# Optimization experiments

Hardware: AMD Instinct MI355X
Metric: run time of the kernel (lower is better)

Reference implementation:

```python
import jax, jax.numpy as jnp
import numpy as np

B, T, C, H = 8, 2048, 1024, 128

def setup_inputs() -> dict:
    key = jax.random.key(0)
    k1, k2, k3, k4 = jax.random.split(key, 4)
    scale = C ** -0.5  # init scale for weights, roughly matches nn.Linear default magnitude
    return {
        "x": jax.random.normal(k1, (B, T, C), dtype=jnp.float32),
        "Wk": jax.random.normal(k2, (C, H), dtype=jnp.float32) * scale,
        "Wq": jax.random.normal(k3, (C, H), dtype=jnp.float32) * scale,
        "Wv": jax.random.normal(k4, (C, H), dtype=jnp.float32) * scale,
    }

def reference(x, Wk, Wq, Wv):
    # x: [B, T, C]; W*: [C, H] (torch Linear weight transposed, bias=False)
    Bx, Tx, Cx = x.shape
    k = x @ Wk  # [B, T, H]
    q = x @ Wq  # [B, T, H]
    v = x @ Wv  # [B, T, H]
    # NOTE: original scales by C**(-0.5) (embedding size), not head_size**-0.5
    scores = jnp.einsum('bth,bsh->bts', q, k) * (Cx ** -0.5)  # [B, T, T]
    causal = jnp.tril(jnp.ones((Tx, Tx), dtype=bool))
    scores = jnp.where(causal, scores, -jnp.inf)
    w = jax.nn.softmax(scores, axis=-1)  # dropout is identity in eval mode
    out = jnp.einsum('bts,bsh->bth', w, v)  # [B, T, H]
    return out
```

## Files before the change

kernel.cpp:

```cpp
#include <hip/hip_runtime.h>


typedef __attribute__((ext_vector_type(8))) short short8;
typedef __attribute__((ext_vector_type(4))) float f32x4;

typedef const __attribute__((address_space(1))) unsigned int* gas_u32p;
typedef __attribute__((address_space(3))) unsigned int* las_u32p;

static __device__ __forceinline__ unsigned short f2bf(float f) {
  unsigned int u = __float_as_uint(f);
  u += 0x7FFF + ((u >> 16) & 1);
  return (unsigned short)(u >> 16);
}

__global__ void wtrans_kernel(const float* __restrict__ Wq,
                              const float* __restrict__ Wk,
                              const float* __restrict__ Wv,
                              unsigned short* __restrict__ Wt) {
  int idx = blockIdx.x * blockDim.x + threadIdx.x;
  int C  = idx >> 3;
  int e  = idx & 7;
  int l  = C & 63;
  int t1 = C >> 6;
  int kh = t1 & 1;
  int t2 = t1 >> 1;
  int w  = t2 % 3;
  int t3 = t2 / 3;
  int wave = t3 & 7;
  int kt   = t3 >> 3;
  int n = wave * 16 + (l & 15);
  int k = kt * 64 + kh * 32 + (l >> 4) * 8 + e;
  const float* W = (w == 0) ? Wq : (w == 1) ? Wk : Wv;
  Wt[idx] = f2bf(W[k * 128 + n]);
}

__global__ __launch_bounds__(512) void qkv_kernel(
    const float* __restrict__ x,
    const unsigned short* __restrict__ Wt,
    unsigned short* __restrict__ q,
    unsigned short* __restrict__ kb,
    unsigned short* __restrict__ vt)
{
  __shared__ float xl[4][4096];
  const int tid  = threadIdx.x;
  const int lane = tid & 63;
  const int wave = tid >> 6;
  const int m0   = blockIdx.x * 64;
  const int lr   = lane & 15;

  f32x4 acc[4][3];
  #pragma unroll
  for (int i = 0; i < 4; ++i)
    #pragma unroll
    for (int w = 0; w < 3; ++w) acc[i][w] = (f32x4){0.f, 0.f, 0.f, 0.f};

  int srow[2], skq[2];
  #pragma unroll
  for (int i = 0; i < 2; ++i) {
    int c  = i * 512 + tid;
    int ln = c & 63;
    int g  = c >> 6;
    srow[i] = (g >> 2) * 16 + (ln & 15);
    skq[i]  = ((g >> 1) & 1) * 8 + (ln >> 4) * 2 + (g & 1);
  }

  #define QSTAGE(KT, BUF)                                                        \
    do {                                                                         \
      _Pragma("unroll")                                                          \
      for (int i = 0; i < 2; ++i) {                                              \
        const float* gsrc = x + (size_t)(m0 + srow[i]) * 1024 + (KT) * 64 + skq[i] * 4; \
        __builtin_amdgcn_global_load_lds((gas_u32p)gsrc,                         \
            (las_u32p)&xl[BUF][(i * 512 + tid) * 4], 16, 0, 0);                  \
      }                                                                          \
    } while (0)

  const unsigned short* w2base = Wt + wave * 3072 + lane * 8;

  #define WLOAD(KT, DST)                                                         \
    do {                                                                         \
      _Pragma("unroll")                                                          \
      for (int w = 0; w < 3; ++w) {                                              \
        DST[w][0] = *reinterpret_cast<const short8*>(w2base + (KT) * 24576 + w * 1024);       \
        DST[w][1] = *reinterpret_cast<const short8*>(w2base + (KT) * 24576 + w * 1024 + 512); \
      }                                                                          \
    } while (0)

  short8 wbuf[2][3][2];

  WLOAD(0, wbuf[0]);
  QSTAGE(0, 0);
  QSTAGE(1, 1);

  #pragma unroll
  for (int kt = 0; kt < 16; ++kt) {
    if (kt < 15) WLOAD(kt + 1, wbuf[(kt + 1) & 1]);
    if (kt < 14) QSTAGE(kt + 2, (kt + 2) & 3);
    if (kt < 14)      asm volatile("s_waitcnt vmcnt(10)" ::: "memory");
    else if (kt < 15) asm volatile("s_waitcnt vmcnt(8)"  ::: "memory");
    else              asm volatile("s_waitcnt vmcnt(0)"  ::: "memory");
    __builtin_amdgcn_sched_barrier(0);
    __builtin_amdgcn_s_barrier();

    short8 af[4][2];
    #pragma unroll
    for (int mf = 0; mf < 4; ++mf)
      #pragma unroll
      for (int kh = 0; kh < 2; ++kh) {
        const float* basep = &xl[kt & 3][((mf * 2 + kh) * 2) * 256 + lane * 4];
        f32x4 h0 = *reinterpret_cast<const f32x4*>(basep);
        f32x4 h1 = *reinterpret_cast<const f32x4*>(basep + 256);
        union { unsigned int w[4]; short8 s; } cv;
        asm("v_cvt_pk_bf16_f32 %0, %1, %2" : "=v"(cv.w[0]) : "v"(h0[0]), "v"(h0[1]));
        asm("v_cvt_pk_bf16_f32 %0, %1, %2" : "=v"(cv.w[1]) : "v"(h0[2]), "v"(h0[3]));
        asm("v_cvt_pk_bf16_f32 %0, %1, %2" : "=v"(cv.w[2]) : "v"(h1[0]), "v"(h1[1]));
        asm("v_cvt_pk_bf16_f32 %0, %1, %2" : "=v"(cv.w[3]) : "v"(h1[2]), "v"(h1[3]));
        af[mf][kh] = cv.s;
      }

    __builtin_amdgcn_s_setprio(1);
    #pragma unroll
    for (int w = 0; w < 3; ++w)
      #pragma unroll
      for (int mf = 0; mf < 4; ++mf) {
        acc[mf][w] = __builtin_amdgcn_mfma_f32_16x16x32_bf16(af[mf][0], wbuf[kt & 1][w][0], acc[mf][w], 0, 0, 0);
        acc[mf][w] = __builtin_amdgcn_mfma_f32_16x16x32_bf16(af[mf][1], wbuf[kt & 1][w][1], acc[mf][w], 0, 0, 0);
      }
    __builtin_amdgcn_s_setprio(0);
  }
  #undef QSTAGE
  #undef WLOAD

  const int h = wave * 16 + lr;
  const int b = m0 >> 11;
  #pragma unroll
  for (int mf = 0; mf < 4; ++mf) {
    int r0 = m0 + mf * 16 + (lane >> 4) * 4;
    #pragma unroll
    for (int j = 0; j < 4; ++j) {
      int r = r0 + j;
      q[(size_t)r * 128 + h] = f2bf(acc[mf][0][j]);
      int rr  = r & 63;
      int nf  = ((rr >> 5) & 1) * 2 + ((rr >> 2) & 1);
      int lrk = ((rr >> 3) & 3) * 4 + (rr & 3);
      size_t kidx = (size_t)(r >> 6) * 8192
                  + (size_t)(((nf * 4 + (h >> 5)) * 64 + ((h >> 3) & 3) * 16 + lrk) * 8 + (h & 7));
      kb[kidx] = f2bf(acc[mf][1][j]);
    }
    int t = r0 & 2047;
    size_t vidx = (size_t)b * 262144 + (size_t)(t >> 6) * 8192
                + (size_t)(((((h >> 4) * 2 + ((t >> 5) & 1)) * 64 + ((t >> 3) & 3) * 16 + (h & 15)) * 8) + (t & 7));
    ushort4 u;
    u.x = f2bf(acc[mf][2][0]); u.y = f2bf(acc[mf][2][1]);
    u.z = f2bf(acc[mf][2][2]); u.w = f2bf(acc[mf][2][3]);
    *reinterpret_cast<ushort4*>(vt + vidx) = u;
  }
}

template<bool MASK>
static __device__ __forceinline__ void body_regs(
    int s, int myrow0, int myrow1, int lg,
    const short8 (&kf)[2][4], const short8 (&vf)[8],
    const short8 (&qf)[2][4], f32x4 (&o)[2][8], float (&lsum)[2])
{
  const float SC = 0.03125f * 1.44269504f;

  f32x4 sT[2][2];
  __builtin_amdgcn_s_setprio(1);
  #pragma unroll
  for (int g = 0; g < 2; ++g)
    #pragma unroll
    for (int nf = 0; nf < 2; ++nf) {
      sT[g][nf] = (f32x4){0.f, 0.f, 0.f, 0.f};
      #pragma unroll
      for (int ks = 0; ks < 4; ++ks)
        sT[g][nf] = __builtin_amdgcn_mfma_f32_16x16x32_bf16(kf[nf][ks], qf[g][ks], sT[g][nf], 0, 0, 0);
    }
  __builtin_amdgcn_s_setprio(0);

  union { unsigned int w[4]; short8 s8; } cv[2];
  #pragma unroll
  for (int g = 0; g < 2; ++g) {
    const int myrow = g ? myrow1 : myrow0;
    float p[8];
    #pragma unroll
    for (int nf = 0; nf < 2; ++nf)
      #pragma unroll
      for (int j = 0; j < 4; ++j) {
        float sv = sT[g][nf][j] * SC;
        if (MASK) {
          int kv = s * 32 + lg * 8 + nf * 4 + j;
          if (kv > myrow) sv = -1e30f;
        }
        p[nf * 4 + j] = exp2f(sv);
      }
    lsum[g] += ((p[0] + p[1]) + (p[2] + p[3])) + ((p[4] + p[5]) + (p[6] + p[7]));
    #pragma unroll
    for (int u = 0; u < 4; ++u)
      asm("v_cvt_pk_bf16_f32 %0, %1, %2" : "=v"(cv[g].w[u]) : "v"(p[u * 2]), "v"(p[u * 2 + 1]));
  }

  __builtin_amdgcn_s_setprio(1);
  #pragma unroll
  for (int g = 0; g < 2; ++g)
    #pragma unroll
    for (int n = 0; n < 8; ++n)
      o[g][n] = __builtin_amdgcn_mfma_f32_16x16x32_bf16(vf[n], cv[g].s8, o[g][n], 0, 0, 0);
  __builtin_amdgcn_s_setprio(0);
}

__global__ __launch_bounds__(256, 2) void attn_kernel(
    const unsigned short* __restrict__ q,
    const unsigned short* __restrict__ kb,
    const unsigned short* __restrict__ vt,
    float* __restrict__ out)
{
  __shared__ float mb[12672];

  const int tid  = threadIdx.x;
  const int lane = tid & 63;
  const int wv   = tid >> 6;
  const int lr = lane & 15;
  const int lg = lane >> 4;
  const int bid = blockIdx.x;
  const int b  = bid & 7;
  const int g2 = bid >> 3;
  const int tt = (g2 < 32) ? (63 - g2) : (g2 - 32);
  const int t0 = tt * 32;
  const int nb = tt + 1;

  const unsigned short* kbase = kb + (size_t)b * 262144;
  const unsigned short* vbase = vt + (size_t)b * 262144;
  const int myrow0 = t0 + lr;
  const int myrow1 = t0 + 16 + lr;

  short8 qf[2][4];
  #pragma unroll
  for (int g = 0; g < 2; ++g) {
    const unsigned short* qp = q + ((size_t)(b * 2048) + (g ? myrow1 : myrow0)) * 128 + lg * 8;
    #pragma unroll
    for (int ks = 0; ks < 4; ++ks)
      qf[g][ks] = *reinterpret_cast<const short8*>(qp + ks * 32);
  }

  f32x4 o[2][8];
  #pragma unroll
  for (int g = 0; g < 2; ++g)
    #pragma unroll
    for (int n = 0; n < 8; ++n) o[g][n] = (f32x4){0.f, 0.f, 0.f, 0.f};
  float lsum[2] = {0.f, 0.f};

  #define GLOADK(KF, S)                                                          \
    do {                                                                         \
      const unsigned short* kg = kbase + (size_t)((S) >> 1) * 8192 + ((S) & 1) * 4096; \
      _Pragma("unroll")                                                          \
      for (int nf = 0; nf < 2; ++nf)                                             \
        _Pragma("unroll")                                                        \
        for (int ks = 0; ks < 4; ++ks)                                           \
          KF[nf][ks] = *reinterpret_cast<const short8*>(kg + ((nf * 4 + ks) * 64 + lane) * 8); \
    } while (0)

  #define GLOADV(S)                                                              \
    do {                                                                         \
      const unsigned short* vg = vbase + (size_t)((S) >> 1) * 8192;              \
      const int hh = (S) & 1;                                                    \
      _Pragma("unroll")                                                          \
      for (int n = 0; n < 8; ++n)                                                \
        vf[n] = *reinterpret_cast<const short8*>(vg + ((n * 2 + hh) * 64 + lane) * 8); \
    } while (0)

  short8 kfA[2][4], kfB[2][4], vf[8];

  if (wv < nb) GLOADK(kfA, wv);

  #define PHASE(CURK, NXTK)                                                      \
    do {                                                                         \
      GLOADV(s);                                                                 \
      if (s + 4 < nb) GLOADK(NXTK, s + 4);                                       \
      if (s == nb - 1)                                                           \
        body_regs<true >(s, myrow0, myrow1, lg, CURK, vf, qf, o, lsum);          \
      else                                                                       \
        body_regs<false>(s, myrow0, myrow1, lg, CURK, vf, qf, o, lsum);          \
    } while (0)

  int s = wv;
  #pragma unroll 1
  while (s < nb) {
    PHASE(kfA, kfB);
    s += 4;
    if (s >= nb) break;
    PHASE(kfB, kfA);
    s += 4;
  }
  #undef PHASE
  #undef GLOADK
  #undef GLOADV

  __syncthreads();
  if (wv != 0) {
    #pragma unroll
    for (int g = 0; g < 2; ++g)
      #pragma unroll
      for (int n = 0; n < 8; ++n) {
        float4 st;
        st.x = o[g][n][0]; st.y = o[g][n][1]; st.z = o[g][n][2]; st.w = o[g][n][3];
        *reinterpret_cast<float4*>(&mb[(size_t)((wv - 1) * 16 + g * 8 + n) * 256 + lane * 4]) = st;
      }
    mb[12288 + (wv - 1) * 128 + lane]      = lsum[0];
    mb[12288 + (wv - 1) * 128 + 64 + lane] = lsum[1];
  }
  __syncthreads();
  if (wv == 0) {
    #pragma unroll
    for (int g = 0; g < 2; ++g) {
      #pragma unroll
      for (int n = 0; n < 8; ++n) {
        #pragma unroll
        for (int w = 1; w < 4; ++w) {
          float4 ad = *reinterpret_cast<const float4*>(
              &mb[(size_t)((w - 1) * 16 + g * 8 + n) * 256 + lane * 4]);
          o[g][n][0] += ad.x; o[g][n][1] += ad.y; o[g][n][2] += ad.z; o[g][n][3] += ad.w;
        }
      }
      float ps = lsum[g];
      #pragma unroll
      for (int w = 1; w < 4; ++w)
        ps += mb[12288 + (w - 1) * 128 + g * 64 + lane];
      ps += __shfl_xor(ps, 16);
      ps += __shfl_xor(ps, 32);
      float rcp = 1.0f / ps;
      float* op = out + ((size_t)(b * 2048) + (g ? myrow1 : myrow0)) * 128;
      #pragma unroll
      for (int n = 0; n < 8; ++n) {
        float4 st;
        st.x = o[g][n][0] * rcp; st.y = o[g][n][1] * rcp;
        st.z = o[g][n][2] * rcp; st.w = o[g][n][3] * rcp;
        *reinterpret_cast<float4*>(op + n * 16 + lg * 4) = st;
      }
    }
  }
}

extern "C" void kernel_launch(void* const* d_in, const int* in_sizes, int n_in,
                              void* d_out, int out_size, void* d_ws, size_t ws_size,
                              hipStream_t stream) {
  const float* x  = (const float*)d_in[0];
  const float* Wk = (const float*)d_in[1];
  const float* Wq = (const float*)d_in[2];
  const float* Wv = (const float*)d_in[3];
  float* out = (float*)d_out;

  char* ws = (char*)d_ws;
  unsigned short* q  = (unsigned short*)(ws);
  unsigned short* kb = (unsigned short*)(ws + (4u  << 20));
  unsigned short* vt = (unsigned short*)(ws + (8u  << 20));
  unsigned short* Wt = (unsigned short*)(ws + (12u << 20));

  wtrans_kernel<<<dim3(1536), dim3(256), 0, stream>>>(Wq, Wk, Wv, Wt);
  qkv_kernel<<<dim3(256), dim3(512), 0, stream>>>(x, Wt, q, kb, vt);
  attn_kernel<<<dim3(512), dim3(256), 0, stream>>>(q, kb, vt, out);
}
```

Before: 57.54 us.

## Process 64-key blocks per wave iteration and drop K double-buffer prefetch

```diff
diff --git a/kernel.cpp b/kernel.cpp
--- a/kernel.cpp
+++ b/kernel.cpp
@@ -157,19 +157,19 @@
 }
 
 template<bool MASK>
-static __device__ __forceinline__ void body_regs(
+static __device__ __forceinline__ void body64(
     int s, int myrow0, int myrow1, int lg,
-    const short8 (&kf)[2][4], const short8 (&vf)[8],
+    const short8 (&kf)[4][4], const short8 (&vf)[8][2],
     const short8 (&qf)[2][4], f32x4 (&o)[2][8], float (&lsum)[2])
 {
   const float SC = 0.03125f * 1.44269504f;
 
-  f32x4 sT[2][2];
+  f32x4 sT[2][4];
   __builtin_amdgcn_s_setprio(1);
   #pragma unroll
   for (int g = 0; g < 2; ++g)
     #pragma unroll
-    for (int nf = 0; nf < 2; ++nf) {
+    for (int nf = 0; nf < 4; ++nf) {
       sT[g][nf] = (f32x4){0.f, 0.f, 0.f, 0.f};
       #pragma unroll
       for (int ks = 0; ks < 4; ++ks)
@@ -177,34 +177,46 @@
     }
   __builtin_amdgcn_s_setprio(0);
 
-  union { unsigned int w[4]; short8 s8; } cv[2];
+  unsigned int pk[2][8];
   #pragma unroll
   for (int g = 0; g < 2; ++g) {
     const int myrow = g ? myrow1 : myrow0;
-    float p[8];
-    #pragma unroll
-    for (int nf = 0; nf < 2; ++nf)
+    float p[16];
+    #pragma unroll
+    for (int nf = 0; nf < 4; ++nf)
       #pragma unroll
       for (int j = 0; j < 4; ++j) {
         float sv = sT[g][nf][j] * SC;
         if (MASK) {
-          int kv = s * 32 + lg * 8 + nf * 4 + j;
+          int kv = s * 64 + (nf >> 1) * 32 + lg * 8 + (nf & 1) * 4 + j;
           if (kv > myrow) sv = -1e30f;
         }
         p[nf * 4 + j] = exp2f(sv);
       }
-    lsum[g] += ((p[0] + p[1]) + (p[2] + p[3])) + ((p[4] + p[5]) + (p[6] + p[7]));
-    #pragma unroll
-    for (int u = 0; u < 4; ++u)
-      asm("v_cvt_pk_bf16_f32 %0, %1, %2" : "=v"(cv[g].w[u]) : "v"(p[u * 2]), "v"(p[u * 2 + 1]));
+    {
+      float s0 = (p[0] + p[1]) + (p[2] + p[3]);
+      float s1 = (p[4] + p[5]) + (p[6] + p[7]);
+      float s2 = (p[8] + p[9]) + (p[10] + p[11]);
+      float s3 = (p[12] + p[13]) + (p[14] + p[15]);
+      lsum[g] += (s0 + s1) + (s2 + s3);
+    }
+    #pragma unroll
+    for (int u = 0; u < 8; ++u)
+      asm("v_cvt_pk_bf16_f32 %0, %1, %2" : "=v"(pk[g][u]) : "v"(p[u * 2]), "v"(p[u * 2 + 1]));
   }
 
   __builtin_amdgcn_s_setprio(1);
   #pragma unroll
-  for (int g = 0; g < 2; ++g)
-    #pragma unroll
-    for (int n = 0; n < 8; ++n)
-      o[g][n] = __builtin_amdgcn_mfma_f32_16x16x32_bf16(vf[n], cv[g].s8, o[g][n], 0, 0, 0);
+  for (int ks = 0; ks < 2; ++ks)
+    #pragma unroll
+    for (int g = 0; g < 2; ++g) {
+      union { unsigned int w[4]; short8 s8; } cv;
+      cv.w[0] = pk[g][ks * 4 + 0]; cv.w[1] = pk[g][ks * 4 + 1];
+      cv.w[2] = pk[g][ks * 4 + 2]; cv.w[3] = pk[g][ks * 4 + 3];
+      #pragma unroll
+      for (int n = 0; n < 8; ++n)
+        o[g][n] = __builtin_amdgcn_mfma_f32_16x16x32_bf16(vf[n][ks], cv.s8, o[g][n], 0, 0, 0);
+    }
   __builtin_amdgcn_s_setprio(0);
 }
 
@@ -226,7 +238,7 @@
   const int g2 = bid >> 3;
   const int tt = (g2 < 32) ? (63 - g2) : (g2 - 32);
   const int t0 = tt * 32;
-  const int nb = tt + 1;
+  const int nb = (tt >> 1) + 1;
 
   const unsigned short* kbase = kb + (size_t)b * 262144;
   const unsigned short* vbase = vt + (size_t)b * 262144;
@@ -249,51 +261,29 @@
     for (int n = 0; n < 8; ++n) o[g][n] = (f32x4){0.f, 0.f, 0.f, 0.f};
   float lsum[2] = {0.f, 0.f};
 
-  #define GLOADK(KF, S)                                                          \
-    do {                                                                         \
-      const unsigned short* kg = kbase + (size_t)((S) >> 1) * 8192 + ((S) & 1) * 4096; \
-      _Pragma("unroll")                                                          \
-      for (int nf = 0; nf < 2; ++nf)                                             \
-        _Pragma("unroll")                                                        \
-        for (int ks = 0; ks < 4; ++ks)                                           \
-          KF[nf][ks] = *reinterpret_cast<const short8*>(kg + ((nf * 4 + ks) * 64 + lane) * 8); \
-    } while (0)
-
-  #define GLOADV(S)                                                              \
-    do {                                                                         \
-      const unsigned short* vg = vbase + (size_t)((S) >> 1) * 8192;              \
-      const int hh = (S) & 1;                                                    \
-      _Pragma("unroll")                                                          \
-      for (int n = 0; n < 8; ++n)                                                \
-        vf[n] = *reinterpret_cast<const short8*>(vg + ((n * 2 + hh) * 64 + lane) * 8); \
-    } while (0)
-
-  short8 kfA[2][4], kfB[2][4], vf[8];
-
-  if (wv < nb) GLOADK(kfA, wv);
-
-  #define PHASE(CURK, NXTK)                                                      \
-    do {                                                                         \
-      GLOADV(s);                                                                 \
-      if (s + 4 < nb) GLOADK(NXTK, s + 4);                                       \
-      if (s == nb - 1)                                                           \
-        body_regs<true >(s, myrow0, myrow1, lg, CURK, vf, qf, o, lsum);          \
-      else                                                                       \
-        body_regs<false>(s, myrow0, myrow1, lg, CURK, vf, qf, o, lsum);          \
-    } while (0)
-
-  int s = wv;
+  short8 kf[4][4], vf[8][2];
+
   #pragma unroll 1
-  while (s < nb) {
-    PHASE(kfA, kfB);
-    s += 4;
-    if (s >= nb) break;
-    PHASE(kfB, kfA);
-    s += 4;
-  }
-  #undef PHASE
-  #undef GLOADK
-  #undef GLOADV
+  for (int s = wv; s < nb; s += 4) {
+    {
+      const unsigned short* kg = kbase + (size_t)s * 8192;
+      const unsigned short* vg = vbase + (size_t)s * 8192;
+      #pragma unroll
+      for (int nf = 0; nf < 4; ++nf)
+        #pragma unroll
+        for (int ks = 0; ks < 4; ++ks)
+          kf[nf][ks] = *reinterpret_cast<const short8*>(kg + ((nf * 4 + ks) * 64 + lane) * 8);
+      #pragma unroll
+      for (int n = 0; n < 8; ++n)
+        #pragma unroll
+        for (int ks = 0; ks < 2; ++ks)
+          vf[n][ks] = *reinterpret_cast<const short8*>(vg + ((n * 2 + ks) * 64 + lane) * 8);
+    }
+    if (s == nb - 1)
+      body64<true >(s, myrow0, myrow1, lg, kf, vf, qf, o, lsum);
+    else
+      body64<false>(s, myrow0, myrow1, lg, kf, vf, qf, o, lsum);
+  }
 
   __syncthreads();
   if (wv != 0) {
```

New measurement: 55.61 us, median of 2. -3.4%, faster.
